# Performance work log

Measured on AMD Instinct MI355X. Metric: run time of the kernel, lower is better.

The kernel has to match this reference:

```python
import jax, jax.numpy as jnp
import numpy as np

EPS = 1e-5  # nn.BatchNorm1d default eps


def setup_inputs() -> dict:
    key = jax.random.key(0)
    ks = jax.random.split(key, 8)
    N_NODES, N_EDGES = 50000, 800000
    D_NODE, D_EDGE, HID, NCLS = 128, 64, 256, 8
    D_IN = D_EDGE + 2 * D_NODE  # 320
    return {
        "n_feats": jax.random.normal(ks[0], (N_NODES, D_NODE), dtype=jnp.float32),
        "edge_feats": jax.random.normal(ks[1], (N_EDGES, D_EDGE), dtype=jnp.float32),
        "src_idx": jax.random.randint(ks[2], (N_EDGES,), 0, N_NODES, dtype=jnp.int64),
        "dst_idx": jax.random.randint(ks[3], (N_EDGES,), 0, N_NODES, dtype=jnp.int64),
        "W1": jax.random.normal(ks[4], (HID, D_IN), dtype=jnp.float32) * (1.0 / np.sqrt(D_IN)),
        "b1": jnp.zeros((HID,), dtype=jnp.float32),
        "gamma": jnp.ones((HID,), dtype=jnp.float32),
        "beta": jnp.zeros((HID,), dtype=jnp.float32),
        "W2": jax.random.normal(ks[5], (NCLS, HID), dtype=jnp.float32) * (1.0 / np.sqrt(HID)),
        "b2": jnp.zeros((NCLS,), dtype=jnp.float32),
    }


def reference(n_feats, edge_feats, src_idx, dst_idx, W1, b1, gamma, beta, W2, b2):
    # gather-concat: [E, d_edge + 2*d_node]
    h = jnp.concatenate([edge_feats, n_feats[src_idx], n_feats[dst_idx]], axis=1)
    # Linear 1
    z = jnp.einsum("ei,hi->eh", h, W1) + b1
    # BatchNorm1d in training mode: batch mean / biased variance over edges
    mu = jnp.mean(z, axis=0)
    var = jnp.mean(jnp.square(z - mu), axis=0)
    zn = (z - mu) * jax.lax.rsqrt(var + EPS) * gamma + beta
    # Linear 2 + LogSoftmax(dim=1)
    logits = jnp.einsum("eh,ch->ec", zn, W2) + b2
    return jax.nn.log_softmax(logits, axis=1)
```

## Files before the change

kernel.cpp:

```cpp
#include <hip/hip_runtime.h>
#include <hip/hip_bf16.h>


#define N_EDGES 800000
#define N_NODES 50000

typedef __attribute__((ext_vector_type(8))) short short8;
typedef __attribute__((ext_vector_type(4))) float f32x4;

#define WS_SUM   0
#define WS_SQ    16384
#define WS_CVEC  32768
#define WS_FLAG  32832
#define WS_MBIG  33280
#define WS_MB    43520
#define WS_MF    45568
#define WS_W1B   55808
#define WS_PS    262144
#define WS_PD    2097152
#define WS_NFB   4194304
#define WS_FAST_NEED (4u << 20)
#define WS_BIG_NEED  16994304u

__device__ __forceinline__ ushort f2bf(float f) {
    union { float f; unsigned int u; } x; x.f = f;
    unsigned int r = x.u + 0x7FFFu + ((x.u >> 16) & 1u);
    return (ushort)(r >> 16);
}
__device__ __forceinline__ short8 cvt8(const float* __restrict__ p) {
    short8 r;
    #pragma unroll
    for (int i = 0; i < 8; i++) r[i] = (short)f2bf(p[i]);
    return r;
}
__device__ __forceinline__ short8 cvtpair(uint4 a, uint4 b) {
    unsigned int v[8] = {a.x, a.y, a.z, a.w, b.x, b.y, b.z, b.w};
    short8 r;
    #pragma unroll
    for (int i = 0; i < 8; i++) {
        unsigned int u = v[i];
        unsigned int rr = u + 0x7FFFu + ((u >> 16) & 1u);
        r[i] = (short)(rr >> 16);
    }
    return r;
}

__device__ __forceinline__ int aidx(int s, int r, int c) {
    return ((s * 128 + r) * 4 + (c ^ ((r >> 1) & 3))) * 8;
}

__global__ void detect_kernel(const int* __restrict__ src,
                              const int* __restrict__ dst, int* flag) {
    int t = threadIdx.x;
    int v = src[2 * t + 1] | dst[2 * t + 1];
    #pragma unroll
    for (int o = 32; o >= 1; o >>= 1) v |= __shfl_xor(v, o);
    if (t == 0) *flag = (v == 0) ? 1 : 0;
}

__global__ __launch_bounds__(256) void prep_kernel(const float* __restrict__ W1,
                                                   ushort* __restrict__ W1b) {
    const int i = (blockIdx.x * 256 + threadIdx.x) * 4;
    const float4 v = *(const float4*)(W1 + i);
    ushort4 o;
    o.x = f2bf(v.x); o.y = f2bf(v.y); o.z = f2bf(v.z); o.w = f2bf(v.w);
    *(ushort4*)(W1b + i) = o;
}

__global__ __launch_bounds__(256) void prep_all_kernel(
    const float* __restrict__ nf, const float* __restrict__ W1,
    const int* __restrict__ src, const int* __restrict__ dst,
    ushort* __restrict__ nfb, ushort* __restrict__ W1b,
    float* __restrict__ zreg, int* __restrict__ flag)
{
    const int t = threadIdx.x;
    const int b = blockIdx.x;
    if (b < 3125) {
        const long i = (long)b * 2048 + t * 8;
        const float4 v0 = *(const float4*)(nf + i);
        const float4 v1 = *(const float4*)(nf + i + 4);
        short8 o;
        o[0] = (short)f2bf(v0.x); o[1] = (short)f2bf(v0.y);
        o[2] = (short)f2bf(v0.z); o[3] = (short)f2bf(v0.w);
        o[4] = (short)f2bf(v1.x); o[5] = (short)f2bf(v1.y);
        o[6] = (short)f2bf(v1.z); o[7] = (short)f2bf(v1.w);
        *(short8*)(nfb + i) = o;
    } else if (b < 3205) {
        const int i = (b - 3125) * 1024 + t * 4;
        const float4 v = *(const float4*)(W1 + i);
        ushort4 o;
        o.x = f2bf(v.x); o.y = f2bf(v.y); o.z = f2bf(v.z); o.w = f2bf(v.w);
        *(ushort4*)(W1b + i) = o;
    } else {
        for (int i = t; i < 8320; i += 256) zreg[i] = 0.f;
        __syncthreads();
        if (t < 64) {
            int v = src[2 * t + 1] | dst[2 * t + 1];
            #pragma unroll
            for (int o = 32; o >= 1; o >>= 1) v |= __shfl_xor(v, o);
            if (t == 0) *flag = (v == 0) ? 1 : 0;
        }
    }
}

template <bool NFB>
__global__ __launch_bounds__(512, 4) void gemm1_stats_kernel(
    const float* __restrict__ nf, const ushort* __restrict__ nfb,
    const float* __restrict__ ef,
    const int* __restrict__ src, const int* __restrict__ dst,
    const ushort* __restrict__ W1b, const int* __restrict__ flag,
    float* __restrict__ g_sum, float* __restrict__ g_sq)
{
    __shared__ ushort a_lds[10 * 128 * 32];

    const int t    = threadIdx.x;
    const int lane = t & 63;
    const int wave = t >> 6;
    const int quad = lane >> 4;
    const int l15  = lane & 15;

    const int wide = *flag;
    const int r     = t >> 2;
    const int chunk = t & 3;
    const long e   = (long)blockIdx.x * 128 + r;
    const int si = src[e << wide], di = dst[e << wide];
    const float* pe = ef + e * 64;

    uint4 efu[2][2];
    #pragma unroll
    for (int s = 0; s < 2; s++) {
        const float* p = pe + s * 32 + chunk * 8;
        efu[s][0] = *(const uint4*)p;
        efu[s][1] = *(const uint4*)(p + 4);
    }

    const ushort* wbase = W1b + (wave * 32 + l15) * 320 + quad * 8;
    short8 bpre[3][2];
    #pragma unroll
    for (int in = 0; in < 2; in++)
        bpre[0][in] = *(const short8*)(wbase + in * 16 * 320);
    #pragma unroll
    for (int in = 0; in < 2; in++)
        bpre[1][in] = *(const short8*)(wbase + in * 16 * 320 + 32);

    if constexpr (NFB) {
        const ushort* psb = nfb + (long)si * 128 + chunk * 8;
        const ushort* pdb = nfb + (long)di * 128 + chunk * 8;
        short8 g[8];
        #pragma unroll
        for (int i = 0; i < 4; i++) g[i]     = *(const short8*)(psb + i * 32);
        #pragma unroll
        for (int i = 0; i < 4; i++) g[4 + i] = *(const short8*)(pdb + i * 32);
        #pragma unroll
        for (int s = 0; s < 2; s++)
            *(short8*)&a_lds[aidx(s, r, chunk)] = cvtpair(efu[s][0], efu[s][1]);
        #pragma unroll
        for (int i = 0; i < 8; i++)
            *(short8*)&a_lds[aidx(2 + i, r, chunk)] = g[i];
    } else {
        const float* ps = nf + (long)si * 128 + chunk * 8;
        const float* pd = nf + (long)di * 128 + chunk * 8;
        uint4 pn[16];
        #pragma unroll
        for (int i = 0; i < 4; i++) {
            pn[i * 2]     = *(const uint4*)(ps + i * 32);
            pn[i * 2 + 1] = *(const uint4*)(ps + i * 32 + 4);
        }
        #pragma unroll
        for (int i = 0; i < 4; i++) {
            pn[8 + i * 2]     = *(const uint4*)(pd + i * 32);
            pn[8 + i * 2 + 1] = *(const uint4*)(pd + i * 32 + 4);
        }
        #pragma unroll
        for (int s = 0; s < 2; s++)
            *(short8*)&a_lds[aidx(s, r, chunk)] = cvtpair(efu[s][0], efu[s][1]);
        #pragma unroll
        for (int i = 0; i < 8; i++)
            *(short8*)&a_lds[aidx(2 + i, r, chunk)] =
                cvtpair(pn[i * 2], pn[i * 2 + 1]);
    }
    __syncthreads();

    f32x4 acc[8][2];
    #pragma unroll
    for (int mb = 0; mb < 8; mb++)
        #pragma unroll
        for (int in = 0; in < 2; in++)
            acc[mb][in] = (f32x4){0.f, 0.f, 0.f, 0.f};

    #pragma unroll
    for (int ks = 0; ks < 10; ks++) {
        if (ks < 8) {
            #pragma unroll
            for (int in = 0; in < 2; in++)
                bpre[(ks + 2) % 3][in] =
                    *(const short8*)(wbase + in * 16 * 320 + (ks + 2) * 32);
        }
        __builtin_amdgcn_s_setprio(1);
        #pragma unroll
        for (int mb = 0; mb < 8; mb++) {
            short8 afr = *(const short8*)
                &a_lds[aidx(ks, mb * 16 + l15, quad)];
            #pragma unroll
            for (int in = 0; in < 2; in++)
                acc[mb][in] = __builtin_amdgcn_mfma_f32_16x16x32_bf16(
                    afr, bpre[ks % 3][in], acc[mb][in], 0, 0, 0);
        }
        __builtin_amdgcn_s_setprio(0);
    }

    const int slot = blockIdx.x & 15;
    #pragma unroll
    for (int in = 0; in < 2; in++) {
        const int col = wave * 32 + in * 16 + l15;
        float s = 0.f, q = 0.f;
        #pragma unroll
        for (int mb = 0; mb < 8; mb++)
            #pragma unroll
            for (int j = 0; j < 4; j++) {
                float v = acc[mb][in][j];
                s += v; q += v * v;
            }
        s += __shfl_xor(s, 16); s += __shfl_xor(s, 32);
        q += __shfl_xor(q, 16); q += __shfl_xor(q, 32);
        if (quad == 0) {
            atomicAdd(&g_sum[slot * 256 + col], s);
            atomicAdd(&g_sq[slot * 256 + col], q);
        }
    }
}

__global__ __launch_bounds__(256) void fold_kernel(
    const float* __restrict__ gamma, const float* __restrict__ beta,
    const float* __restrict__ W1, const float* __restrict__ b1,
    const float* __restrict__ W2, const float* __restrict__ b2,
    const float* __restrict__ g_sum, const float* __restrict__ g_sq,
    ushort* __restrict__ Mbig, ushort* __restrict__ Mb,
    float* __restrict__ Mf, float* __restrict__ Cvec)
{
    __shared__ float a_sh[256][8];
    __shared__ float red[8];
    __shared__ float mk_sh[64][8];
    const int t = threadIdx.x;

    float ssum = 0.f, ssq = 0.f;
    #pragma unroll
    for (int s = 0; s < 16; s++) {
        ssum += g_sum[s * 256 + t];
        ssq  += g_sq[s * 256 + t];
    }
    const float invE   = 1.0f / (float)N_EDGES;
    const float mu_acc = ssum * invE;
    float var = ssq * invE - mu_acc * mu_acc;
    var = fmaxf(var, 0.f);
    const float b1v = b1[t];
    const float mu  = mu_acc + b1v;
    const float g   = gamma[t] * rsqrtf(var + 1e-5f);
    const float sh  = b1v * g + beta[t] - mu * g;

    if (t < 8) red[t] = 0.f;
    ((float*)mk_sh)[t] = 0.f;
    ((float*)mk_sh)[t + 256] = 0.f;
    __syncthreads();
    #pragma unroll
    for (int c = 0; c < 8; c++) {
        const float w = W2[c * 256 + t];
        a_sh[t][c] = w * g;
        if (blockIdx.x == 0) atomicAdd(&red[c], w * sh);
    }
    __syncthreads();

    const int k  = blockIdx.x * 64 + (t & 63);
    const int q4 = t >> 6;
    float m[8] = {0.f, 0.f, 0.f, 0.f, 0.f, 0.f, 0.f, 0.f};
    #pragma unroll 8
    for (int hh = q4 * 64; hh < q4 * 64 + 64; hh++) {
        const float w1 = W1[hh * 320 + k];
        #pragma unroll
        for (int c = 0; c < 8; c++) m[c] += a_sh[hh][c] * w1;
    }
    #pragma unroll
    for (int c = 0; c < 8; c++) atomicAdd(&mk_sh[t & 63][c], m[c]);
    __syncthreads();

    if (t < 64) {
        const int kk = blockIdx.x * 64 + t;
        #pragma unroll
        for (int c = 0; c < 8; c++) {
            const float mv = mk_sh[t][c];
            Mf[c * 320 + kk]   = mv;
            Mbig[c * 320 + kk] = f2bf(mv);
            if (kk < 64) Mb[c * 64 + kk] = f2bf(mv);
        }
        #pragma unroll
        for (int c = 8; c < 16; c++) {
            Mbig[c * 320 + kk] = 0;
            if (kk < 64) Mb[c * 64 + kk] = 0;
        }
    }
    if (blockIdx.x == 0) {
        if (t < 8)       Cvec[t] = b2[t] + red[t];
        else if (t < 16) Cvec[t] = 0.f;
    }
}

__global__ __launch_bounds__(256) void fold_nodeproj_kernel(
    const float* __restrict__ gamma, const float* __restrict__ beta,
    const float* __restrict__ W1, const float* __restrict__ b1,
    const float* __restrict__ W2, const float* __restrict__ b2,
    const float* __restrict__ g_sum, const float* __restrict__ g_sq,
    const float* __restrict__ nf, ushort* __restrict__ Mb,
    float* __restrict__ Cvec, float* __restrict__ Ps, float* __restrict__ Pd)
{
    __shared__ float a_sh[256][8];
    __shared__ float red[8];
    __shared__ float Ms[8][128];
    __shared__ float Md[8][128];
    const int t = threadIdx.x;

    float ssum = 0.f, ssq = 0.f;
    #pragma unroll
    for (int s = 0; s < 16; s++) {
        ssum += g_sum[s * 256 + t];
        ssq  += g_sq[s * 256 + t];
    }
    const float invE   = 1.0f / (float)N_EDGES;
    const float mu_acc = ssum * invE;
    float var = ssq * invE - mu_acc * mu_acc;
    var = fmaxf(var, 0.f);
    const float b1v = b1[t];
    const float mu  = mu_acc + b1v;
    const float g   = gamma[t] * rsqrtf(var + 1e-5f);
    const float sh  = b1v * g + beta[t] - mu * g;

    if (t < 8) red[t] = 0.f;
    __syncthreads();
    #pragma unroll
    for (int c = 0; c < 8; c++) {
        const float w = W2[c * 256 + t];
        a_sh[t][c] = w * g;
        if (blockIdx.x == 0) atomicAdd(&red[c], w * sh);
    }
    __syncthreads();

    float m[8] = {0.f, 0.f, 0.f, 0.f, 0.f, 0.f, 0.f, 0.f};
    #pragma unroll 8
    for (int hh = 0; hh < 256; hh++) {
        const float w1 = W1[hh * 320 + 64 + t];
        #pragma unroll
        for (int c = 0; c < 8; c++) m[c] += a_sh[hh][c] * w1;
    }
    #pragma unroll
    for (int c = 0; c < 8; c++) {
        if (t < 128) Ms[c][t] = m[c];
        else         Md[c][t - 128] = m[c];
    }
    if (blockIdx.x == 0) {
        if (t < 64) {
            float mm[8] = {0.f, 0.f, 0.f, 0.f, 0.f, 0.f, 0.f, 0.f};
            #pragma unroll 8
            for (int hh = 0; hh < 256; hh++) {
                const float w1 = W1[hh * 320 + t];
                #pragma unroll
                for (int c = 0; c < 8; c++) mm[c] += a_sh[hh][c] * w1;
            }
            #pragma unroll
            for (int c = 0; c < 8; c++)  Mb[c * 64 + t] = f2bf(mm[c]);
            #pragma unroll
            for (int c = 8; c < 16; c++) Mb[c * 64 + t] = 0;
        }
        if (t < 8)       Cvec[t] = b2[t] + red[t];
        else if (t < 16) Cvec[t] = 0.f;
    }
    __syncthreads();

    const int n = blockIdx.x * 256 + t;
    if (n >= N_NODES) return;
    float as[8] = {0,0,0,0,0,0,0,0}, ad[8] = {0,0,0,0,0,0,0,0};
    #pragma unroll 4
    for (int k = 0; k < 128; k += 4) {
        const float4 v = *(const float4*)(nf + (long)n * 128 + k);
        #pragma unroll
        for (int c = 0; c < 8; c++) {
            const float4 ms = *(const float4*)&Ms[c][k];
            const float4 md = *(const float4*)&Md[c][k];
            as[c] += v.x * ms.x + v.y * ms.y + v.z * ms.z + v.w * ms.w;
            ad[c] += v.x * md.x + v.y * md.y + v.z * md.z + v.w * md.w;
        }
    }
    #pragma unroll
    for (int c = 0; c < 8; c++) {
        Ps[n * 8 + c] = as[c];
        Pd[n * 8 + c] = ad[c];
    }
}

__global__ __launch_bounds__(256) void nodeproj_kernel(
    const float* __restrict__ nf, const float* __restrict__ Mf,
    float* __restrict__ Ps, float* __restrict__ Pd)
{
    __shared__ float Ms[8][128];
    __shared__ float Md[8][128];
    const int t = threadIdx.x;
    #pragma unroll
    for (int i = 0; i < 4; i++) {
        const int f = t + i * 256;
        Ms[f >> 7][f & 127] = Mf[(f >> 7) * 320 + 64  + (f & 127)];
        Md[f >> 7][f & 127] = Mf[(f >> 7) * 320 + 192 + (f & 127)];
    }
    __syncthreads();
    const int n = blockIdx.x * 256 + t;
    if (n >= N_NODES) return;
    float as[8] = {0,0,0,0,0,0,0,0}, ad[8] = {0,0,0,0,0,0,0,0};
    #pragma unroll 4
    for (int k = 0; k < 128; k += 4) {
        const float4 v = *(const float4*)(nf + (long)n * 128 + k);
        #pragma unroll
        for (int c = 0; c < 8; c++) {
            const float4 ms = *(const float4*)&Ms[c][k];
            const float4 md = *(const float4*)&Md[c][k];
            as[c] += v.x * ms.x + v.y * ms.y + v.z * ms.z + v.w * ms.w;
            ad[c] += v.x * md.x + v.y * md.y + v.z * md.z + v.w * md.w;
        }
    }
    #pragma unroll
    for (int c = 0; c < 8; c++) {
        Ps[n * 8 + c] = as[c];
        Pd[n * 8 + c] = ad[c];
    }
}

__global__ __launch_bounds__(256) void edge_out_kernel(
    const float* __restrict__ ef, const int* __restrict__ src,
    const int* __restrict__ dst, const int* __restrict__ flag,
    const ushort* __restrict__ Mb, const float* __restrict__ Ps,
    const float* __restrict__ Pd, const float* __restrict__ Cvec,
    float* __restrict__ out)
{
    __shared__ float x_sh[4][64][16];
    const int t    = threadIdx.x;
    const int lane = t & 63;
    const int wave = t >> 6;
    const int quad = lane >> 4;
    const int l15  = lane & 15;
    const int wide = *flag;
    const long eb  = (long)blockIdx.x * 256 + wave * 64;

    const long ei = (eb + lane) << wide;
    const int sidx = src[ei], didx = dst[ei];
    const float4 s0 = *(const float4*)(Ps + sidx * 8);
    const float4 s1 = *(const float4*)(Ps + sidx * 8 + 4);
    const float4 d0 = *(const float4*)(Pd + didx * 8);
    const float4 d1 = *(const float4*)(Pd + didx * 8 + 4);
    const float4 c0 = *(const float4*)(Cvec);
    const float4 c1 = *(const float4*)(Cvec + 4);

    uint4 ea[4][2], eb4[4][2];
    #pragma unroll
    for (int mb = 0; mb < 4; mb++)
        #pragma unroll
        for (int ks = 0; ks < 2; ks++) {
            const float* p = ef + (eb + mb * 16 + l15) * 64 + ks * 32 + quad * 8;
            ea[mb][ks]  = *(const uint4*)p;
            eb4[mb][ks] = *(const uint4*)(p + 4);
        }

    f32x4 acc[4];
    #pragma unroll
    for (int mb = 0; mb < 4; mb++) acc[mb] = (f32x4){0.f, 0.f, 0.f, 0.f};

    const ushort* bbase = Mb + l15 * 64 + quad * 8;
    #pragma unroll
    for (int ks = 0; ks < 2; ks++) {
        short8 bfr = *(const short8*)(bbase + ks * 32);
        #pragma unroll
        for (int mb = 0; mb < 4; mb++)
            acc[mb] = __builtin_amdgcn_mfma_f32_16x16x32_bf16(
                cvtpair(ea[mb][ks], eb4[mb][ks]), bfr, acc[mb], 0, 0, 0);
    }

    #pragma unroll
    for (int mb = 0; mb < 4; mb++)
        #pragma unroll
        for (int j = 0; j < 4; j++)
            x_sh[wave][mb * 16 + quad * 4 + j][l15] = acc[mb][j];
    __syncthreads();

    const float4 xa = *(const float4*)&x_sh[wave][lane][0];
    const float4 xb = *(const float4*)&x_sh[wave][lane][4];

    float x0 = xa.x + c0.x + s0.x + d0.x;
    float x1 = xa.y + c0.y + s0.y + d0.y;
    float x2 = xa.z + c0.z + s0.z + d0.z;
    float x3 = xa.w + c0.w + s0.w + d0.w;
    float x4 = xb.x + c1.x + s1.x + d1.x;
    float x5 = xb.y + c1.y + s1.y + d1.y;
    float x6 = xb.z + c1.z + s1.z + d1.z;
    float x7 = xb.w + c1.w + s1.w + d1.w;

    float m = fmaxf(fmaxf(fmaxf(x0, x1), fmaxf(x2, x3)),
                    fmaxf(fmaxf(x4, x5), fmaxf(x6, x7)));
    float sx = __expf(x0 - m) + __expf(x1 - m) + __expf(x2 - m) +
               __expf(x3 - m) + __expf(x4 - m) + __expf(x5 - m) +
               __expf(x6 - m) + __expf(x7 - m);
    const float l = m + __logf(sx);

    float* po = out + (eb + lane) * 8;
    float4 o0 = {x0 - l, x1 - l, x2 - l, x3 - l};
    float4 o1 = {x4 - l, x5 - l, x6 - l, x7 - l};
    *(float4*)po       = o0;
    *(float4*)(po + 4) = o1;
}

__global__ __launch_bounds__(256) void out_kernel(
    const float* __restrict__ nf, const float* __restrict__ ef,
    const int* __restrict__ src, const int* __restrict__ dst,
    const int* __restrict__ flag, const ushort* __restrict__ M,
    const float* __restrict__ Cvec, float* __restrict__ out)
{
    const int t    = threadIdx.x;
    const int lane = t & 63;
    const int wave = t >> 6;
    const int quad = lane >> 4;
    const int l15  = lane & 15;
    const int wide = *flag;
    const long eb  = (long)blockIdx.x * 256 + wave * 64;

    const float* pe[4]; const float* ps[4]; const float* pd[4];
    #pragma unroll
    for (int mb = 0; mb < 4; mb++) {
        const long e  = eb + mb * 16 + l15;
        const int si = src[e << wide], di = dst[e << wide];
        pe[mb] = ef + e * 64;
        ps[mb] = nf + (long)si * 128;
        pd[mb] = nf + (long)di * 128;
    }
    f32x4 acc[4];
    #pragma unroll
    for (int mb = 0; mb < 4; mb++) acc[mb] = (f32x4){0.f, 0.f, 0.f, 0.f};
    const ushort* bbase = M + l15 * 320 + quad * 8;
    #pragma unroll
    for (int ks = 0; ks < 10; ks++) {
        const int k0 = ks * 32;
        short8 bfr = *(const short8*)(bbase + k0);
        const int koff = k0 + quad * 8;
        #pragma unroll
        for (int mb = 0; mb < 4; mb++) {
            const float* p = (ks < 2) ? (pe[mb] + koff)
                           : (ks < 6) ? (ps[mb] + (koff - 64))
                                      : (pd[mb] + (koff - 192));
            acc[mb] = __builtin_amdgcn_mfma_f32_16x16x32_bf16(
                cvt8(p), bfr, acc[mb], 0, 0, 0);
        }
    }
    const float bv = Cvec[l15];
    #pragma unroll
    for (int mb = 0; mb < 4; mb++)
        #pragma unroll
        for (int j = 0; j < 4; j++) {
            float x = acc[mb][j] + bv;
            float m = x;
            m = fmaxf(m, __shfl_xor(m, 1));
            m = fmaxf(m, __shfl_xor(m, 2));
            m = fmaxf(m, __shfl_xor(m, 4));
            float sx = __expf(x - m);
            sx += __shfl_xor(sx, 1);
            sx += __shfl_xor(sx, 2);
            sx += __shfl_xor(sx, 4);
            const float o = x - m - __logf(sx);
            if (l15 < 8)
                out[(eb + mb * 16 + quad * 4 + j) * 8 + l15] = o;
        }
}

extern "C" void kernel_launch(void* const* d_in, const int* in_sizes, int n_in,
                              void* d_out, int out_size, void* d_ws, size_t ws_size,
                              hipStream_t stream) {
    const float* nf    = (const float*)d_in[0];
    const float* ef    = (const float*)d_in[1];
    const int*   src   = (const int*)d_in[2];
    const int*   dst   = (const int*)d_in[3];
    const float* W1    = (const float*)d_in[4];
    const float* b1    = (const float*)d_in[5];
    const float* gamma = (const float*)d_in[6];
    const float* beta  = (const float*)d_in[7];
    const float* W2    = (const float*)d_in[8];
    const float* b2    = (const float*)d_in[9];

    char*   ws    = (char*)d_ws;
    float*  g_sum = (float*)(ws + WS_SUM);
    float*  g_sq  = (float*)(ws + WS_SQ);
    float*  Cvec  = (float*)(ws + WS_CVEC);
    int*    flag  = (int*)(ws + WS_FLAG);
    ushort* Mbig  = (ushort*)(ws + WS_MBIG);
    ushort* Mb    = (ushort*)(ws + WS_MB);
    float*  Mf    = (float*)(ws + WS_MF);
    ushort* W1b   = (ushort*)(ws + WS_W1B);
    float*  Ps    = (float*)(ws + WS_PS);
    float*  Pd    = (float*)(ws + WS_PD);
    ushort* nfb   = (ushort*)(ws + WS_NFB);
    float*  out   = (float*)d_out;

    const bool fast = ws_size >= (size_t)WS_FAST_NEED;
    const bool big  = ws_size >= (size_t)WS_BIG_NEED;

    if (big) {
        prep_all_kernel<<<3206, 256, 0, stream>>>(nf, W1, src, dst, nfb, W1b,
                                                  (float*)ws, flag);
        gemm1_stats_kernel<true><<<N_EDGES / 128, 512, 0, stream>>>(
            nf, nfb, ef, src, dst, W1b, flag, g_sum, g_sq);
        fold_nodeproj_kernel<<<(N_NODES + 255) / 256, 256, 0, stream>>>(
            gamma, beta, W1, b1, W2, b2, g_sum, g_sq, nf, Mb, Cvec, Ps, Pd);
        edge_out_kernel<<<N_EDGES / 256, 256, 0, stream>>>(ef, src, dst, flag,
                                                           Mb, Ps, Pd, Cvec, out);
    } else {
        hipMemsetAsync(ws, 0, 33280, stream);
        detect_kernel<<<1, 64, 0, stream>>>(src, dst, flag);
        prep_kernel<<<80, 256, 0, stream>>>(W1, W1b);
        gemm1_stats_kernel<false><<<N_EDGES / 128, 512, 0, stream>>>(
            nf, nfb, ef, src, dst, W1b, flag, g_sum, g_sq);
        fold_kernel<<<5, 256, 0, stream>>>(gamma, beta, W1, b1, W2, b2,
                                           g_sum, g_sq, Mbig, Mb, Mf, Cvec);
        if (fast) {
            nodeproj_kernel<<<(N_NODES + 255) / 256, 256, 0, stream>>>(nf, Mf, Ps, Pd);
            edge_out_kernel<<<N_EDGES / 256, 256, 0, stream>>>(ef, src, dst, flag,
                                                               Mb, Ps, Pd, Cvec, out);
        } else {
            out_kernel<<<N_EDGES / 256, 256, 0, stream>>>(nf, ef, src, dst, flag,
                                                          Mbig, Cvec, out);
        }
    }
}
```

Baseline: 516.9 us.

## Precompute per-node W1 projections and compute BN stats from gathered projections

```diff
diff --git a/kernel.cpp b/kernel.cpp
--- a/kernel.cpp
+++ b/kernel.cpp
@@ -19,13 +19,20 @@
 #define WS_PS    262144
 #define WS_PD    2097152
 #define WS_NFB   4194304
+#define WS_BT    16994304
+#define WS_CT    42618880
 #define WS_FAST_NEED (4u << 20)
 #define WS_BIG_NEED  16994304u
+#define WS_HUGE_NEED 68243456u
 
 __device__ __forceinline__ ushort f2bf(float f) {
     union { float f; unsigned int u; } x; x.f = f;
     unsigned int r = x.u + 0x7FFFu + ((x.u >> 16) & 1u);
     return (ushort)(r >> 16);
+}
+__device__ __forceinline__ float bf2f(ushort u) {
+    union { unsigned int i; float f; } x; x.i = ((unsigned int)u) << 16;
+    return x.f;
 }
 __device__ __forceinline__ short8 cvt8(const float* __restrict__ p) {
     short8 r;
@@ -103,6 +110,151 @@
     }
 }
 
+__global__ __launch_bounds__(512, 4) void projBC_kernel(
+    const ushort* __restrict__ nfb, const ushort* __restrict__ W1b,
+    ushort* __restrict__ Bt, ushort* __restrict__ Ct)
+{
+    __shared__ ushort a_lds[64 * 128];
+    const int t    = threadIdx.x;
+    const int lane = t & 63;
+    const int wave = t >> 6;
+    const int quad = lane >> 4;
+    const int l15  = lane & 15;
+    const int nb   = blockIdx.x * 64;
+
+    {
+        const int r  = t >> 3;
+        const int cp = (t & 7) * 2;
+        const int rn = min(nb + r, N_NODES - 1);
+        const ushort* p = nfb + (long)rn * 128;
+        short8 v0 = *(const short8*)(p + cp * 8);
+        short8 v1 = *(const short8*)(p + cp * 8 + 8);
+        *(short8*)&a_lds[(r * 16 + (cp ^ (r & 7))) * 8]       = v0;
+        *(short8*)&a_lds[(r * 16 + ((cp + 1) ^ (r & 7))) * 8] = v1;
+    }
+
+    const int hbase = (wave & 3) * 64;
+    const int koff0 = (wave < 4) ? 64 : 192;
+
+    __syncthreads();
+
+    f32x4 acc[4][4];
+    #pragma unroll
+    for (int a = 0; a < 4; a++)
+        #pragma unroll
+        for (int b = 0; b < 4; b++) acc[a][b] = (f32x4){0.f, 0.f, 0.f, 0.f};
+
+    #pragma unroll
+    for (int ks = 0; ks < 4; ks++) {
+        short8 bfr[4];
+        #pragma unroll
+        for (int in = 0; in < 4; in++)
+            bfr[in] = *(const short8*)(W1b + (hbase + in * 16 + l15) * 320 +
+                                       koff0 + ks * 32 + quad * 8);
+        #pragma unroll
+        for (int mb = 0; mb < 4; mb++) {
+            const int r = mb * 16 + l15;
+            short8 afr = *(const short8*)
+                &a_lds[(r * 16 + ((ks * 4 + quad) ^ (r & 7))) * 8];
+            #pragma unroll
+            for (int in = 0; in < 4; in++)
+                acc[mb][in] = __builtin_amdgcn_mfma_f32_16x16x32_bf16(
+                    afr, bfr[in], acc[mb][in], 0, 0, 0);
+        }
+    }
+
+    ushort* __restrict__ tab = (wave < 4) ? Bt : Ct;
+    #pragma unroll
+    for (int mb = 0; mb < 4; mb++)
+        #pragma unroll
+        for (int in = 0; in < 4; in++)
+            #pragma unroll
+            for (int j = 0; j < 4; j++) {
+                const int n = nb + mb * 16 + quad * 4 + j;
+                tab[(long)n * 256 + hbase + in * 16 + l15] =
+                    f2bf(acc[mb][in][j]);
+            }
+}
+
+__global__ __launch_bounds__(256, 4) void stats_kernel(
+    const float* __restrict__ ef, const int* __restrict__ src,
+    const int* __restrict__ dst, const int* __restrict__ flag,
+    const ushort* __restrict__ W1b, const ushort* __restrict__ Bt,
+    const ushort* __restrict__ Ct,
+    float* __restrict__ g_sum, float* __restrict__ g_sq)
+{
+    __shared__ ushort A_sh[64][258];
+    __shared__ int idx_sh[128];
+    const int t    = threadIdx.x;
+    const int lane = t & 63;
+    const int wave = t >> 6;
+    const int quad = lane >> 4;
+    const int l15  = lane & 15;
+    const int wide = *flag;
+    const long eb  = (long)blockIdx.x * 64;
+
+    if (t < 128) {
+        const int e = t & 63;
+        const long ei = (eb + e) << wide;
+        idx_sh[t] = (t < 64) ? src[ei] : dst[ei];
+    }
+
+    f32x4 acc[4][4];
+    #pragma unroll
+    for (int a = 0; a < 4; a++)
+        #pragma unroll
+        for (int b = 0; b < 4; b++) acc[a][b] = (f32x4){0.f, 0.f, 0.f, 0.f};
+
+    #pragma unroll
+    for (int ks = 0; ks < 2; ks++) {
+        short8 bfr[4];
+        #pragma unroll
+        for (int in = 0; in < 4; in++)
+            bfr[in] = *(const short8*)(W1b + (wave * 64 + in * 16 + l15) * 320 +
+                                       ks * 32 + quad * 8);
+        #pragma unroll
+        for (int mb = 0; mb < 4; mb++) {
+            const float* p = ef + (eb + mb * 16 + l15) * 64 + ks * 32 + quad * 8;
+            uint4 a = *(const uint4*)p;
+            uint4 b = *(const uint4*)(p + 4);
+            short8 afr = cvtpair(a, b);
+            #pragma unroll
+            for (int in = 0; in < 4; in++)
+                acc[mb][in] = __builtin_amdgcn_mfma_f32_16x16x32_bf16(
+                    afr, bfr[in], acc[mb][in], 0, 0, 0);
+        }
+    }
+
+    #pragma unroll
+    for (int mb = 0; mb < 4; mb++)
+        #pragma unroll
+        for (int in = 0; in < 4; in++)
+            #pragma unroll
+            for (int j = 0; j < 4; j++)
+                A_sh[mb * 16 + quad * 4 + j][wave * 64 + in * 16 + l15] =
+                    f2bf(acc[mb][in][j]);
+    __syncthreads();
+
+    const int c = t;
+    const ushort* __restrict__ pB = Bt + c;
+    const ushort* __restrict__ pC = Ct + c;
+    float sum = 0.f, sq = 0.f;
+    #pragma unroll 8
+    for (int e = 0; e < 64; e++) {
+        const int s = idx_sh[e];
+        const int d = idx_sh[64 + e];
+        const float bv = bf2f(pB[(long)s * 256]);
+        const float cv = bf2f(pC[(long)d * 256]);
+        const float av = bf2f(A_sh[e][c]);
+        const float z = av + bv + cv;
+        sum += z;
+        sq = fmaf(z, z, sq);
+    }
+    const int slot = blockIdx.x & 15;
+    atomicAdd(&g_sum[slot * 256 + c], sum);
+    atomicAdd(&g_sq[slot * 256 + c], sq);
+}
+
 template <bool NFB>
 __global__ __launch_bounds__(512, 4) void gemm1_stats_kernel(
     const float* __restrict__ nf, const ushort* __restrict__ nfb,
@@ -599,12 +751,25 @@
     float*  Ps    = (float*)(ws + WS_PS);
     float*  Pd    = (float*)(ws + WS_PD);
     ushort* nfb   = (ushort*)(ws + WS_NFB);
+    ushort* Bt    = (ushort*)(ws + WS_BT);
+    ushort* Ct    = (ushort*)(ws + WS_CT);
     float*  out   = (float*)d_out;
 
     const bool fast = ws_size >= (size_t)WS_FAST_NEED;
     const bool big  = ws_size >= (size_t)WS_BIG_NEED;
-
-    if (big) {
+    const bool huge = ws_size >= (size_t)WS_HUGE_NEED;
+
+    if (huge) {
+        prep_all_kernel<<<3206, 256, 0, stream>>>(nf, W1, src, dst, nfb, W1b,
+                                                  (float*)ws, flag);
+        projBC_kernel<<<782, 512, 0, stream>>>(nfb, W1b, Bt, Ct);
+        stats_kernel<<<N_EDGES / 64, 256, 0, stream>>>(ef, src, dst, flag,
+                                                       W1b, Bt, Ct, g_sum, g_sq);
+        fold_nodeproj_kernel<<<(N_NODES + 255) / 256, 256, 0, stream>>>(
+            gamma, beta, W1, b1, W2, b2, g_sum, g_sq, nf, Mb, Cvec, Ps, Pd);
+        edge_out_kernel<<<N_EDGES / 256, 256, 0, stream>>>(ef, src, dst, flag,
+                                                           Mb, Ps, Pd, Cvec, out);
+    } else if (big) {
         prep_all_kernel<<<3206, 256, 0, stream>>>(nf, W1, src, dst, nfb, W1b,
                                                   (float*)ws, flag);
         gemm1_stats_kernel<true><<<N_EDGES / 128, 512, 0, stream>>>(
```

After: 628.0 us. 21.5% more time.
